# Kernel optimization log

Measured on AMD Instinct MI355X. Metric: run time of the kernel, lower is better.

## Reference

```python
import jax, jax.numpy as jnp
import numpy as np

N = 16384      # nodes
E = 524288     # edges (avg degree 32)
D = 128        # node_dim
H = 256        # hidden_dim
C = 10         # num_classes
G = 64         # graphs in batch


def setup_inputs() -> dict:
    key = jax.random.key(0)
    ks = jax.random.split(key, 8)
    x = jax.random.normal(ks[0], (N, D), dtype=jnp.float32)
    edge_index = jax.random.randint(ks[1], (2, E), 0, N)
    batch = jnp.sort(jax.random.randint(ks[2], (N,), 0, G))
    s = 0.05
    W1 = jax.random.normal(ks[3], (D, H), dtype=jnp.float32) * s
    b1 = jnp.zeros((H,), dtype=jnp.float32)
    W2 = jax.random.normal(ks[4], (H, H), dtype=jnp.float32) * s
    b2 = jnp.zeros((H,), dtype=jnp.float32)
    Wc = jax.random.normal(ks[5], (H, C), dtype=jnp.float32) * s
    bc = jnp.zeros((C,), dtype=jnp.float32)
    return {"x": x, "edge_index": edge_index, "batch": batch,
            "W1": W1, "b1": b1, "W2": W2, "b2": b2, "Wc": Wc, "bc": bc}


def _adj_norm(edge_index, n, dtype):
    # dense adjacency with self-loops (duplicates collapse to 1 via .set),
    # symmetric degree normalization D^{-1/2} A D^{-1/2}
    adj = jnp.zeros((n, n), dtype=dtype)
    adj = adj.at[edge_index[0], edge_index[1]].set(1.0)
    diag = jnp.arange(n)
    adj = adj.at[diag, diag].set(1.0)
    deg = jnp.clip(adj.sum(axis=1), 1.0, None)
    dis = deg ** -0.5
    return dis[:, None] * adj * dis[None, :]


def reference(x, edge_index, batch, W1, b1, W2, b2, Wc, bc):
    n = x.shape[0]
    A = _adj_norm(edge_index, n, x.dtype)   # [n, n], same for both layers
    h = jax.nn.relu((A @ x) @ W1 + b1)      # GCN layer 1 + relu
    h = jax.nn.relu((A @ h) @ W2 + b2)      # GCN layer 2 + relu
    pooled = jax.ops.segment_sum(h, batch, num_segments=G)            # [G, H]
    counts = jax.ops.segment_sum(jnp.ones((n,), h.dtype), batch, num_segments=G)
    pooled = pooled / jnp.clip(counts, 1.0, None)[:, None]
    # dropout is identity in eval mode
    return pooled @ Wc + bc                  # [G, C]
```

## Files before the change

kernel.cpp:

```cpp
#include <hip/hip_runtime.h>
#include <hip/hip_fp16.h>

#define NN 16384
#define EE 524288
#define DDIM 128
#define HDIM 256
#define CDIM 10
#define GG 64
#define MAXD 128

typedef _Float16 h8 __attribute__((ext_vector_type(8)));
typedef float f4 __attribute__((ext_vector_type(4)));
typedef unsigned short su8 __attribute__((ext_vector_type(8)));

#define OFF_XH   0ull
#define OFF_ELL  4194304ull
#define OFF_ELLP 8388608ull
#define OFF_Y1H  16777216ull
#define OFF_H1   20971520ull
#define OFF_Y2H  29360128ull
#define OFF_DEG  37748736ull
#define OFF_DIS  37814272ull
#define OFF_POOL 37879808ull
#define OFF_CNT  37945344ull
#define OFF_WT1  37949440ull
#define OFF_WT2  38014976ull

__global__ void init_all(const float* __restrict__ x, _Float16* __restrict__ xh,
                         const float* __restrict__ W1, _Float16* __restrict__ wt1,
                         const float* __restrict__ W2, _Float16* __restrict__ wt2,
                         const int* __restrict__ ei, unsigned short* __restrict__ ell,
                         int* __restrict__ deg,
                         float* __restrict__ pooled, float* __restrict__ cnt,
                         const int* __restrict__ batch) {
    int b = blockIdx.x, t = threadIdx.x;
    if (b < 2048) {
        int i = (b * 256 + t) * 4;
        float4 v = *(const float4*)(x + i);
        _Float16 o[4] = {(_Float16)v.x, (_Float16)v.y, (_Float16)v.z, (_Float16)v.w};
        *(ushort4*)(xh + i) = *(ushort4*)o;
    } else if (b < 2176) {
        int i = (b - 2048) * 256 + t;
        int n = i / DDIM, k = i - n * DDIM;
        wt1[i] = (_Float16)W1[k * 256 + n];
    } else if (b < 2432) {
        int i = (b - 2176) * 256 + t;
        int n = i / HDIM, k = i - n * HDIM;
        wt2[i] = (_Float16)W2[k * 256 + n];
    } else if (b < 2496) {
        int r = (b - 2432) * 256 + t;
        pooled[r] = 0.0f;
        if (r < GG) {
            int lo = 0, hi = NN;
            while (lo < hi) { int m = (lo + hi) >> 1; if (batch[m] < r) lo = m + 1; else hi = m; }
            int a = lo;
            lo = 0; hi = NN;
            while (lo < hi) { int m = (lo + hi) >> 1; if (batch[m] < r + 1) lo = m + 1; else hi = m; }
            cnt[r] = (float)(lo - a);
        }
    } else {
        int e = ((b - 2496) * 256 + t) * 2;
        int2 s2 = *(const int2*)(ei + e);
        int2 d2 = *(const int2*)(ei + EE + e);
        int pos = atomicAdd(&deg[s2.x], 1) + 1;
        if (pos < MAXD) ell[s2.x * MAXD + pos] = (unsigned short)d2.x;
        pos = atomicAdd(&deg[s2.y], 1) + 1;
        if (pos < MAXD) ell[s2.y * MAXD + pos] = (unsigned short)d2.y;
    }
}

__global__ __launch_bounds__(256) void dedup_kernel(unsigned short* __restrict__ ell,
                                                    int* __restrict__ deg,
                                                    float* __restrict__ dis) {
    int row  = blockIdx.x * 4 + (threadIdx.x >> 6);
    int lane = threadIdx.x & 63;
    int d = deg[row] + 1;
    if (d > MAXD) d = MAXD;
    int c0 = (lane == 0) ? row : ell[row * MAXD + lane];
    int c1 = ell[row * MAXD + 64 + lane];
    bool k0 = lane < d;
    bool k1 = (64 + lane) < d;
    for (int j = 0; j < d - 1; j++) {
        int cj0 = __shfl(c0, j & 63, 64);
        int cj1 = __shfl(c1, j & 63, 64);
        int cj = (j < 64) ? cj0 : cj1;
        if (k0 && lane > j && c0 == cj) k0 = false;
        if (k1 && (64 + lane) > j && c1 == cj) k1 = false;
    }
    unsigned long long m0 = __ballot(k0);
    unsigned long long m1 = __ballot(k1);
    int nd = __popcll(m0) + __popcll(m1);
    unsigned long long below = (lane == 0) ? 0ull : ((~0ull) >> (64 - lane));
    int p0 = __popcll(m0 & below);
    int p1 = __popcll(m0) + __popcll(m1 & below);
    if (k0) ell[row * MAXD + p0] = (unsigned short)c0;
    if (k1) ell[row * MAXD + p1] = (unsigned short)c1;
    if (lane == 0) {
        deg[row] = nd;
        dis[row] = 1.0f / sqrtf((float)nd);
    }
}

__global__ void pack_kernel(const unsigned short* __restrict__ ell,
                            const int* __restrict__ deg, const float* __restrict__ dis,
                            unsigned* __restrict__ ellp) {
    int i = blockIdx.x * 256 + threadIdx.x;
    int row = i >> 7;
    int slot = i & 127;
    int c = ell[i] & (NN - 1);
    float w = (slot < deg[row]) ? dis[c] : 0.0f;
    _Float16 wh = (_Float16)w;
    ellp[i] = (unsigned)c | ((unsigned)(*(unsigned short*)&wh) << 16);
}

template <int COLS>
__global__ __launch_bounds__(256) void spmm_f16(const _Float16* __restrict__ src,
                                                const unsigned* __restrict__ ellp,
                                                const int* __restrict__ deg,
                                                const float* __restrict__ dis,
                                                _Float16* __restrict__ y) {
    constexpr int SEG = COLS / 8;
    constexpr int NS  = 64 / SEG;
    constexpr int ST  = 2 * NS;
    __shared__ unsigned scw[2][MAXD];
    __shared__ float red[2][ST][COLS];
    const int row0 = blockIdx.x * 2;
    const int t    = threadIdx.x;
    const int wv   = t >> 6;
    const int ri   = wv >> 1;
    const int wp   = wv & 1;
    const int lane = t & 63;
    const int sid  = lane / SEG;
    const int l    = lane % SEG;
    const int row  = row0 + ri;
    if (t < 2 * MAXD) scw[t >> 7][t & 127] = ellp[(size_t)(row0 + (t >> 7)) * MAXD + (t & 127)];
    __syncthreads();
    const int d    = deg[row];
    const int dpad = (d + ST - 1) & ~(ST - 1);

    float acc[8];
#pragma unroll
    for (int j = 0; j < 8; j++) acc[j] = 0.0f;

    const int stream = wp * NS + sid;
    unsigned ucur = scw[ri][stream];
    su8 hcur = *(const su8*)(src + (size_t)(ucur & 0xFFFF) * COLS + l * 8);
    for (int k = stream; k < dpad; k += ST) {
        const int kn = k + ST;
        unsigned unext = 0;
        su8 hnext;
        if (kn < dpad) {
            unext = scw[ri][kn];
            hnext = *(const su8*)(src + (size_t)(unext & 0xFFFF) * COLS + l * 8);
        }
        unsigned short wb = (unsigned short)(ucur >> 16);
        float wgt = (float)(*(_Float16*)&wb);
#pragma unroll
        for (int j = 0; j < 8; j++) {
            unsigned short hb = hcur[j];
            acc[j] = fmaf(wgt, (float)(*(_Float16*)&hb), acc[j]);
        }
        ucur = unext;
        hcur = hnext;
    }
    *(f4*)&red[ri][stream][l * 8]     = (f4){acc[0], acc[1], acc[2], acc[3]};
    *(f4*)&red[ri][stream][l * 8 + 4] = (f4){acc[4], acc[5], acc[6], acc[7]};
    __syncthreads();
    if (COLS == 256) {
        float s0 = 0.0f, s1 = 0.0f;
#pragma unroll
        for (int q = 0; q < ST; q++) { s0 += red[0][q][t]; s1 += red[1][q][t]; }
        y[(size_t)row0 * COLS + t]       = (_Float16)(dis[row0] * s0);
        y[(size_t)(row0 + 1) * COLS + t] = (_Float16)(dis[row0 + 1] * s1);
    } else {
        int rr = t >> 7, c = t & 127;
        float s = 0.0f;
#pragma unroll
        for (int q = 0; q < ST; q++) s += red[rr][q][c];
        y[(size_t)(row0 + rr) * COLS + c] = (_Float16)(dis[row0 + rr] * s);
    }
}

#define ASTR 40
#define BSTR 40

#define MFMA_PROLOG                                                            \
    const int r0 = blockIdx.x * 128;                                           \
    const int c0 = blockIdx.y * 64;                                            \
    const int t = threadIdx.x;                                                 \
    const int lane = t & 63, wv = t >> 6;                                      \
    const int wm = wv >> 1, wn = wv & 1;                                       \
    const int qm = lane & 15, qk = lane >> 4;                                  \
    f4 acc[4][2];                                                              \
    _Pragma("unroll") for (int i = 0; i < 4; i++)                              \
        _Pragma("unroll") for (int j = 0; j < 2; j++)                          \
            acc[i][j] = (f4){0.f, 0.f, 0.f, 0.f};

#define MFMA_KLOOP(Aptr, Wtptr, K)                                             \
    for (int k0 = 0; k0 < K; k0 += 32) {                                       \
        __syncthreads();                                                       \
        {                                                                      \
            int r = t >> 1, ko = (t & 1) * 16;                                 \
            const su8* srcA = (const su8*)(Aptr + (size_t)(r0 + r) * K + k0 + ko); \
            su8 a0 = srcA[0], a1 = srcA[1];                                    \
            *(su8*)&As[r * ASTR + ko]     = a0;                                \
            *(su8*)&As[r * ASTR + ko + 8] = a1;                                \
            int n = t >> 2, ko2 = (t & 3) * 8;                                 \
            *(su8*)&Bs[n * BSTR + ko2] =                                       \
                *(const su8*)(Wtptr + (size_t)(c0 + n) * K + k0 + ko2);        \
        }                                                                      \
        __syncthreads();                                                       \
        h8 bfr[2];                                                             \
        _Pragma("unroll") for (int j = 0; j < 2; j++)                          \
            bfr[j] = *(const h8*)&Bs[(wn * 32 + j * 16 + qm) * BSTR + qk * 8]; \
        _Pragma("unroll") for (int i = 0; i < 4; i++) {                        \
            h8 afr = *(const h8*)&As[(wm * 64 + i * 16 + qm) * ASTR + qk * 8]; \
            _Pragma("unroll") for (int j = 0; j < 2; j++)                      \
                acc[i][j] = __builtin_amdgcn_mfma_f32_16x16x32_f16(            \
                    afr, bfr[j], acc[i][j], 0, 0, 0);                          \
        }                                                                      \
    }

template <int K>
__global__ __launch_bounds__(256) void gemm_mfma_f16(
        const _Float16* __restrict__ A, const _Float16* __restrict__ Wt,
        const float* __restrict__ bias, _Float16* __restrict__ H) {
    __shared__ __align__(16) _Float16 As[128 * ASTR];
    __shared__ __align__(16) _Float16 Bs[64 * BSTR];
    __shared__ __align__(16) _Float16 Cs[128 * 72];
    MFMA_PROLOG
    MFMA_KLOOP(A, Wt, K)

    float bv[2];
#pragma unroll
    for (int j = 0; j < 2; j++) bv[j] = bias[c0 + wn * 32 + j * 16 + qm];
#pragma unroll
    for (int i = 0; i < 4; i++)
#pragma unroll
        for (int j = 0; j < 2; j++) {
            int lc = wn * 32 + j * 16 + qm;
#pragma unroll
            for (int rr = 0; rr < 4; rr++) {
                int lr = wm * 64 + i * 16 + qk * 4 + rr;
                Cs[lr * 72 + lc] = (_Float16)fmaxf(acc[i][j][rr] + bv[j], 0.0f);
            }
        }
    __syncthreads();
    {
        int r = t >> 1, half_ = t & 1;
        _Float16* dst = H + (size_t)(r0 + r) * 256 + c0 + half_ * 32;
        const _Float16* srcc = &Cs[r * 72 + half_ * 32];
#pragma unroll
        for (int q = 0; q < 4; q++)
            *(su8*)(dst + q * 8) = *(const su8*)(srcc + q * 8);
    }
}

#define NG 8
template <int K>
__global__ __launch_bounds__(256) void gemm_mfma_pool(
        const _Float16* __restrict__ A, const _Float16* __restrict__ Wt,
        const float* __restrict__ bias, const int* __restrict__ batch,
        float* __restrict__ pooled) {
    __shared__ __align__(16) _Float16 As[128 * ASTR];
    __shared__ __align__(16) _Float16 Bs[64 * BSTR];
    __shared__ float pools[NG][68];
    __shared__ int sb[128];
    MFMA_PROLOG
    if (t < 128) sb[t] = batch[r0 + t];
    for (int i = t; i < NG * 68; i += 256) ((float*)pools)[i] = 0.0f;
    MFMA_KLOOP(A, Wt, K)

    float bv[2];
#pragma unroll
    for (int j = 0; j < 2; j++) bv[j] = bias[c0 + wn * 32 + j * 16 + qm];
    __syncthreads();
    const int g0 = sb[0];
#pragma unroll
    for (int i = 0; i < 4; i++)
#pragma unroll
        for (int j = 0; j < 2; j++) {
            int lc = wn * 32 + j * 16 + qm;
#pragma unroll
            for (int rr = 0; rr < 4; rr++) {
                int lr = wm * 64 + i * 16 + qk * 4 + rr;
                int gi = min(sb[lr] - g0, NG - 1);
                float v = fmaxf(acc[i][j][rr] + bv[j], 0.0f);
                atomicAdd(&pools[gi][lc], v);
            }
        }
    __syncthreads();
    const int ng = min(sb[127] - g0 + 1, NG);
    for (int i2 = t; i2 < ng * 64; i2 += 256) {
        int gi = i2 >> 6, c = i2 & 63;
        float v = pools[gi][c];
        if (v != 0.0f) atomicAdd(&pooled[(g0 + gi) * 256 + c0 + c], v);
    }
}

__global__ void head_kernel(const float* __restrict__ pooled,
                            const float* __restrict__ cnt,
                            const float* __restrict__ Wc,
                            const float* __restrict__ bc,
                            float* __restrict__ out) {
    int g = blockIdx.x;
    int l = threadIdx.x;
    float inv = 1.0f / fmaxf(cnt[g], 1.0f);
    float acc[CDIM];
#pragma unroll
    for (int c = 0; c < CDIM; c++) acc[c] = 0.0f;
    for (int t = l; t < 256; t += 64) {
        float pv = pooled[g * 256 + t] * inv;
#pragma unroll
        for (int c = 0; c < CDIM; c++) acc[c] = fmaf(pv, Wc[t * CDIM + c], acc[c]);
    }
#pragma unroll
    for (int c = 0; c < CDIM; c++) {
        float v = acc[c];
        for (int off = 32; off > 0; off >>= 1) v += __shfl_down(v, off, 64);
        if (l == 0) out[g * CDIM + c] = v + bc[c];
    }
}

extern "C" void kernel_launch(void* const* d_in, const int* in_sizes, int n_in,
                              void* d_out, int out_size, void* d_ws, size_t ws_size,
                              hipStream_t stream) {
    const float* x  = (const float*)d_in[0];
    const int*   ei = (const int*)d_in[1];
    const int*   batch = (const int*)d_in[2];
    const float* W1 = (const float*)d_in[3];
    const float* b1 = (const float*)d_in[4];
    const float* W2 = (const float*)d_in[5];
    const float* b2 = (const float*)d_in[6];
    const float* Wc = (const float*)d_in[7];
    const float* bc = (const float*)d_in[8];
    float* out = (float*)d_out;

    char* ws = (char*)d_ws;
    _Float16* xh   = (_Float16*)(ws + OFF_XH);
    unsigned short* ell = (unsigned short*)(ws + OFF_ELL);
    unsigned* ellp = (unsigned*)(ws + OFF_ELLP);
    _Float16* y1h  = (_Float16*)(ws + OFF_Y1H);
    _Float16* h1   = (_Float16*)(ws + OFF_H1);
    _Float16* y2h  = (_Float16*)(ws + OFF_Y2H);
    int*   deg     = (int*)(ws + OFF_DEG);
    float* dis     = (float*)(ws + OFF_DIS);
    float* pooled  = (float*)(ws + OFF_POOL);
    float* cnt     = (float*)(ws + OFF_CNT);
    _Float16* wt1  = (_Float16*)(ws + OFF_WT1);
    _Float16* wt2  = (_Float16*)(ws + OFF_WT2);

    hipMemsetAsync(deg, 0, NN * sizeof(int), stream);
    init_all<<<3520, 256, 0, stream>>>(x, xh, W1, wt1, W2, wt2, ei, ell, deg,
                                       pooled, cnt, batch);
    dedup_kernel<<<NN / 4, 256, 0, stream>>>(ell, deg, dis);
    pack_kernel<<<(NN * MAXD) / 256, 256, 0, stream>>>(ell, deg, dis, ellp);
    spmm_f16<DDIM><<<NN / 2, 256, 0, stream>>>(xh, ellp, deg, dis, y1h);
    {
        dim3 grid(NN / 128, 256 / 64);
        gemm_mfma_f16<DDIM><<<grid, 256, 0, stream>>>(y1h, wt1, b1, h1);
    }
    spmm_f16<HDIM><<<NN / 2, 256, 0, stream>>>(h1, ellp, deg, dis, y2h);
    {
        dim3 grid(NN / 128, 256 / 64);
        gemm_mfma_pool<HDIM><<<grid, 256, 0, stream>>>(y2h, wt2, b2, batch, pooled);
    }
    head_kernel<<<GG, 64, 0, stream>>>(pooled, cnt, Wc, bc, out);
}
```

Before: 217.0 us.

## Fuse sparse aggregation with MFMA GEMM per layer into single kernels

Each GCN layer's sparse gather (SpMM) and its dense MFMA GEMM now run in one kernel. Each 512-thread block gathers 32 aggregated rows into shared memory, then multiplies them by the full weight matrix and applies bias and ReLU. Layer 2 also fuses the mean-pool atomics. This removes the y1h/y2h intermediate round-trips through global memory and two kernel launches. In exchange, the gather changes from a two-wave, software-pipelined scheme to one wave per row with shuffle reductions and no prefetch, and every block reloads the full weight matrix.

```diff
diff --git a/kernel.cpp b/kernel.cpp
--- a/kernel.cpp
+++ b/kernel.cpp
@@ -16,15 +16,13 @@
 #define OFF_XH   0ull
 #define OFF_ELL  4194304ull
 #define OFF_ELLP 8388608ull
-#define OFF_Y1H  16777216ull
-#define OFF_H1   20971520ull
-#define OFF_Y2H  29360128ull
-#define OFF_DEG  37748736ull
-#define OFF_DIS  37814272ull
-#define OFF_POOL 37879808ull
-#define OFF_CNT  37945344ull
-#define OFF_WT1  37949440ull
-#define OFF_WT2  38014976ull
+#define OFF_H1   16777216ull
+#define OFF_DEG  25165824ull
+#define OFF_DIS  25231360ull
+#define OFF_POOL 25296896ull
+#define OFF_CNT  25362432ull
+#define OFF_WT1  25366528ull
+#define OFF_WT2  25432064ull
 
 __global__ void init_all(const float* __restrict__ x, _Float16* __restrict__ xh,
                          const float* __restrict__ W1, _Float16* __restrict__ wt1,
@@ -113,188 +111,179 @@
     ellp[i] = (unsigned)c | ((unsigned)(*(unsigned short*)&wh) << 16);
 }
 
-template <int COLS>
-__global__ __launch_bounds__(256) void spmm_f16(const _Float16* __restrict__ src,
-                                                const unsigned* __restrict__ ellp,
-                                                const int* __restrict__ deg,
-                                                const float* __restrict__ dis,
-                                                _Float16* __restrict__ y) {
-    constexpr int SEG = COLS / 8;
+template <int KK, int YSTR, int RPW>
+__device__ __forceinline__ void gather_rows(const _Float16* __restrict__ src,
+                                            const unsigned* __restrict__ ellp,
+                                            const int* __restrict__ deg,
+                                            const float* __restrict__ dis,
+                                            _Float16* ytile, int r0, int t) {
+    constexpr int SEG = KK / 8;
     constexpr int NS  = 64 / SEG;
-    constexpr int ST  = 2 * NS;
-    __shared__ unsigned scw[2][MAXD];
-    __shared__ float red[2][ST][COLS];
-    const int row0 = blockIdx.x * 2;
-    const int t    = threadIdx.x;
-    const int wv   = t >> 6;
-    const int ri   = wv >> 1;
-    const int wp   = wv & 1;
-    const int lane = t & 63;
-    const int sid  = lane / SEG;
-    const int l    = lane % SEG;
-    const int row  = row0 + ri;
-    if (t < 2 * MAXD) scw[t >> 7][t & 127] = ellp[(size_t)(row0 + (t >> 7)) * MAXD + (t & 127)];
+    const int wv = t >> 6, lane = t & 63;
+    const int sid = lane / SEG, l = lane % SEG;
+    for (int rr = 0; rr < RPW; rr++) {
+        const int rowl = wv * RPW + rr;
+        const int row = r0 + rowl;
+        unsigned c0 = ellp[row * MAXD + lane];
+        unsigned c1 = ellp[row * MAXD + 64 + lane];
+        const int d = deg[row];
+        const int dpad = (d + NS - 1) & ~(NS - 1);
+        float acc[8];
+#pragma unroll
+        for (int j = 0; j < 8; j++) acc[j] = 0.0f;
+        for (int k = sid; k < dpad; k += NS) {
+            unsigned ua = __shfl(c0, k & 63, 64);
+            unsigned ub = __shfl(c1, k & 63, 64);
+            unsigned u = (k < 64) ? ua : ub;
+            unsigned short wb = (unsigned short)(u >> 16);
+            float wgt = (float)(*(_Float16*)&wb);
+            su8 hv = *(const su8*)(src + (size_t)(u & 0xFFFF) * KK + l * 8);
+#pragma unroll
+            for (int j = 0; j < 8; j++) {
+                unsigned short hb = hv[j];
+                acc[j] = fmaf(wgt, (float)(*(_Float16*)&hb), acc[j]);
+            }
+        }
+        if (SEG == 16) {
+#pragma unroll
+            for (int j = 0; j < 8; j++) acc[j] += __shfl_xor(acc[j], 16, 64);
+        }
+#pragma unroll
+        for (int j = 0; j < 8; j++) acc[j] += __shfl_xor(acc[j], 32, 64);
+        if (lane < SEG) {
+            float dr = dis[row];
+            _Float16 o[8];
+#pragma unroll
+            for (int j = 0; j < 8; j++) o[j] = (_Float16)(dr * acc[j]);
+            *(su8*)&ytile[rowl * YSTR + l * 8] = *(su8*)o;
+        }
+    }
+}
+
+#define BSTR 40
+
+__global__ __launch_bounds__(512) void fused_layer1(
+        const _Float16* __restrict__ xh, const unsigned* __restrict__ ellp,
+        const int* __restrict__ deg, const float* __restrict__ dis,
+        const _Float16* __restrict__ Wt, const float* __restrict__ bias,
+        _Float16* __restrict__ H) {
+    __shared__ __align__(16) _Float16 ytile[32 * 136];
+    __shared__ __align__(16) _Float16 Bs[256 * BSTR];
+    const int r0 = blockIdx.x * 32;
+    const int t = threadIdx.x;
+    gather_rows<DDIM, 136, 4>(xh, ellp, deg, dis, ytile, r0, t);
+
+    const int lane = t & 63, wv = t >> 6;
+    const int wm = wv >> 2, wn = wv & 3;
+    const int qm = lane & 15, qk = lane >> 4;
+    f4 acc[4];
+#pragma unroll
+    for (int j = 0; j < 4; j++) acc[j] = (f4){0.f, 0.f, 0.f, 0.f};
+
+    for (int k0 = 0; k0 < DDIM; k0 += 32) {
+        __syncthreads();
+        {
+            int n = t >> 1, ko = (t & 1) * 16;
+            *(su8*)&Bs[n * BSTR + ko]     = *(const su8*)(Wt + (size_t)n * DDIM + k0 + ko);
+            *(su8*)&Bs[n * BSTR + ko + 8] = *(const su8*)(Wt + (size_t)n * DDIM + k0 + ko + 8);
+        }
+        __syncthreads();
+        h8 afr = *(const h8*)&ytile[(wm * 16 + qm) * 136 + k0 + qk * 8];
+#pragma unroll
+        for (int j = 0; j < 4; j++) {
+            h8 bfr = *(const h8*)&Bs[(wn * 64 + j * 16 + qm) * BSTR + qk * 8];
+            acc[j] = __builtin_amdgcn_mfma_f32_16x16x32_f16(afr, bfr, acc[j], 0, 0, 0);
+        }
+    }
+
+    float bv[4];
+#pragma unroll
+    for (int j = 0; j < 4; j++) bv[j] = bias[wn * 64 + j * 16 + qm];
+
+#pragma unroll
+    for (int pass = 0; pass < 2; pass++) {
+        __syncthreads();
+        if ((wn >> 1) == pass) {
+            int lc = (wn & 1) * 64;
+#pragma unroll
+            for (int j = 0; j < 4; j++) {
+#pragma unroll
+                for (int rr = 0; rr < 4; rr++) {
+                    int lr = wm * 16 + qk * 4 + rr;
+                    ytile[lr * 136 + lc + j * 16 + qm] =
+                        (_Float16)fmaxf(acc[j][rr] + bv[j], 0.0f);
+                }
+            }
+        }
+        __syncthreads();
+        {
+            int row = t >> 4, cg = (t & 15) * 8;
+            *(su8*)(H + (size_t)(r0 + row) * 256 + pass * 128 + cg) =
+                *(const su8*)&ytile[row * 136 + cg];
+        }
+    }
+}
+
+#define NG 8
+__global__ __launch_bounds__(512) void fused_layer2(
+        const _Float16* __restrict__ h1, const unsigned* __restrict__ ellp,
+        const int* __restrict__ deg, const float* __restrict__ dis,
+        const _Float16* __restrict__ Wt, const float* __restrict__ bias,
+        const int* __restrict__ batch, float* __restrict__ pooled) {
+    __shared__ __align__(16) _Float16 ytile[32 * 264];
+    __shared__ __align__(16) _Float16 Bs[256 * BSTR];
+    __shared__ float pools[NG * 264];
+    __shared__ int sb[32];
+    const int r0 = blockIdx.x * 32;
+    const int t = threadIdx.x;
+    if (t < 32) sb[t] = batch[r0 + t];
+    for (int i = t; i < NG * 264; i += 512) pools[i] = 0.0f;
+    gather_rows<HDIM, 264, 4>(h1, ellp, deg, dis, ytile, r0, t);
+
+    const int lane = t & 63, wv = t >> 6;
+    const int wm = wv >> 2, wn = wv & 3;
+    const int qm = lane & 15, qk = lane >> 4;
+    f4 acc[4];
+#pragma unroll
+    for (int j = 0; j < 4; j++) acc[j] = (f4){0.f, 0.f, 0.f, 0.f};
+
+    for (int k0 = 0; k0 < HDIM; k0 += 32) {
+        __syncthreads();
+        {
+            int n = t >> 1, ko = (t & 1) * 16;
+            *(su8*)&Bs[n * BSTR + ko]     = *(const su8*)(Wt + (size_t)n * HDIM + k0 + ko);
+            *(su8*)&Bs[n * BSTR + ko + 8] = *(const su8*)(Wt + (size_t)n * HDIM + k0 + ko + 8);
+        }
+        __syncthreads();
+        h8 afr = *(const h8*)&ytile[(wm * 16 + qm) * 264 + k0 + qk * 8];
+#pragma unroll
+        for (int j = 0; j < 4; j++) {
+            h8 bfr = *(const h8*)&Bs[(wn * 64 + j * 16 + qm) * BSTR + qk * 8];
+            acc[j] = __builtin_amdgcn_mfma_f32_16x16x32_f16(afr, bfr, acc[j], 0, 0, 0);
+        }
+    }
+
+    float bv[4];
+#pragma unroll
+    for (int j = 0; j < 4; j++) bv[j] = bias[wn * 64 + j * 16 + qm];
+    const int g0 = sb[0];
+#pragma unroll
+    for (int j = 0; j < 4; j++) {
+        int lc = wn * 64 + j * 16 + qm;
+#pragma unroll
+        for (int rr = 0; rr < 4; rr++) {
+            int lr = wm * 16 + qk * 4 + rr;
+            int gi = min(sb[lr] - g0, NG - 1);
+            float v = fmaxf(acc[j][rr] + bv[j], 0.0f);
+            atomicAdd(&pools[gi * 264 + lc], v);
+        }
+    }
     __syncthreads();
-    const int d    = deg[row];
-    const int dpad = (d + ST - 1) & ~(ST - 1);
-
-    float acc[8];
-#pragma unroll
-    for (int j = 0; j < 8; j++) acc[j] = 0.0f;
-
-    const int stream = wp * NS + sid;
-    unsigned ucur = scw[ri][stream];
-    su8 hcur = *(const su8*)(src + (size_t)(ucur & 0xFFFF) * COLS + l * 8);
-    for (int k = stream; k < dpad; k += ST) {
-        const int kn = k + ST;
-        unsigned unext = 0;
-        su8 hnext;
-        if (kn < dpad) {
-            unext = scw[ri][kn];
-            hnext = *(const su8*)(src + (size_t)(unext & 0xFFFF) * COLS + l * 8);
-        }
-        unsigned short wb = (unsigned short)(ucur >> 16);
-        float wgt = (float)(*(_Float16*)&wb);
-#pragma unroll
-        for (int j = 0; j < 8; j++) {
-            unsigned short hb = hcur[j];
-            acc[j] = fmaf(wgt, (float)(*(_Float16*)&hb), acc[j]);
-        }
-        ucur = unext;
-        hcur = hnext;
-    }
-    *(f4*)&red[ri][stream][l * 8]     = (f4){acc[0], acc[1], acc[2], acc[3]};
-    *(f4*)&red[ri][stream][l * 8 + 4] = (f4){acc[4], acc[5], acc[6], acc[7]};
-    __syncthreads();
-    if (COLS == 256) {
-        float s0 = 0.0f, s1 = 0.0f;
-#pragma unroll
-        for (int q = 0; q < ST; q++) { s0 += red[0][q][t]; s1 += red[1][q][t]; }
-        y[(size_t)row0 * COLS + t]       = (_Float16)(dis[row0] * s0);
-        y[(size_t)(row0 + 1) * COLS + t] = (_Float16)(dis[row0 + 1] * s1);
-    } else {
-        int rr = t >> 7, c = t & 127;
-        float s = 0.0f;
-#pragma unroll
-        for (int q = 0; q < ST; q++) s += red[rr][q][c];
-        y[(size_t)(row0 + rr) * COLS + c] = (_Float16)(dis[row0 + rr] * s);
-    }
-}
-
-#define ASTR 40
-#define BSTR 40
-
-#define MFMA_PROLOG                                                            \
-    const int r0 = blockIdx.x * 128;                                           \
-    const int c0 = blockIdx.y * 64;                                            \
-    const int t = threadIdx.x;                                                 \
-    const int lane = t & 63, wv = t >> 6;                                      \
-    const int wm = wv >> 1, wn = wv & 1;                                       \
-    const int qm = lane & 15, qk = lane >> 4;                                  \
-    f4 acc[4][2];                                                              \
-    _Pragma("unroll") for (int i = 0; i < 4; i++)                              \
-        _Pragma("unroll") for (int j = 0; j < 2; j++)                          \
-            acc[i][j] = (f4){0.f, 0.f, 0.f, 0.f};
-
-#define MFMA_KLOOP(Aptr, Wtptr, K)                                             \
-    for (int k0 = 0; k0 < K; k0 += 32) {                                       \
-        __syncthreads();                                                       \
-        {                                                                      \
-            int r = t >> 1, ko = (t & 1) * 16;                                 \
-            const su8* srcA = (const su8*)(Aptr + (size_t)(r0 + r) * K + k0 + ko); \
-            su8 a0 = srcA[0], a1 = srcA[1];                                    \
-            *(su8*)&As[r * ASTR + ko]     = a0;                                \
-            *(su8*)&As[r * ASTR + ko + 8] = a1;                                \
-            int n = t >> 2, ko2 = (t & 3) * 8;                                 \
-            *(su8*)&Bs[n * BSTR + ko2] =                                       \
-                *(const su8*)(Wtptr + (size_t)(c0 + n) * K + k0 + ko2);        \
-        }                                                                      \
-        __syncthreads();                                                       \
-        h8 bfr[2];                                                             \
-        _Pragma("unroll") for (int j = 0; j < 2; j++)                          \
-            bfr[j] = *(const h8*)&Bs[(wn * 32 + j * 16 + qm) * BSTR + qk * 8]; \
-        _Pragma("unroll") for (int i = 0; i < 4; i++) {                        \
-            h8 afr = *(const h8*)&As[(wm * 64 + i * 16 + qm) * ASTR + qk * 8]; \
-            _Pragma("unroll") for (int j = 0; j < 2; j++)                      \
-                acc[i][j] = __builtin_amdgcn_mfma_f32_16x16x32_f16(            \
-                    afr, bfr[j], acc[i][j], 0, 0, 0);                          \
-        }                                                                      \
-    }
-
-template <int K>
-__global__ __launch_bounds__(256) void gemm_mfma_f16(
-        const _Float16* __restrict__ A, const _Float16* __restrict__ Wt,
-        const float* __restrict__ bias, _Float16* __restrict__ H) {
-    __shared__ __align__(16) _Float16 As[128 * ASTR];
-    __shared__ __align__(16) _Float16 Bs[64 * BSTR];
-    __shared__ __align__(16) _Float16 Cs[128 * 72];
-    MFMA_PROLOG
-    MFMA_KLOOP(A, Wt, K)
-
-    float bv[2];
-#pragma unroll
-    for (int j = 0; j < 2; j++) bv[j] = bias[c0 + wn * 32 + j * 16 + qm];
-#pragma unroll
-    for (int i = 0; i < 4; i++)
-#pragma unroll
-        for (int j = 0; j < 2; j++) {
-            int lc = wn * 32 + j * 16 + qm;
-#pragma unroll
-            for (int rr = 0; rr < 4; rr++) {
-                int lr = wm * 64 + i * 16 + qk * 4 + rr;
-                Cs[lr * 72 + lc] = (_Float16)fmaxf(acc[i][j][rr] + bv[j], 0.0f);
-            }
-        }
-    __syncthreads();
-    {
-        int r = t >> 1, half_ = t & 1;
-        _Float16* dst = H + (size_t)(r0 + r) * 256 + c0 + half_ * 32;
-        const _Float16* srcc = &Cs[r * 72 + half_ * 32];
-#pragma unroll
-        for (int q = 0; q < 4; q++)
-            *(su8*)(dst + q * 8) = *(const su8*)(srcc + q * 8);
-    }
-}
-
-#define NG 8
-template <int K>
-__global__ __launch_bounds__(256) void gemm_mfma_pool(
-        const _Float16* __restrict__ A, const _Float16* __restrict__ Wt,
-        const float* __restrict__ bias, const int* __restrict__ batch,
-        float* __restrict__ pooled) {
-    __shared__ __align__(16) _Float16 As[128 * ASTR];
-    __shared__ __align__(16) _Float16 Bs[64 * BSTR];
-    __shared__ float pools[NG][68];
-    __shared__ int sb[128];
-    MFMA_PROLOG
-    if (t < 128) sb[t] = batch[r0 + t];
-    for (int i = t; i < NG * 68; i += 256) ((float*)pools)[i] = 0.0f;
-    MFMA_KLOOP(A, Wt, K)
-
-    float bv[2];
-#pragma unroll
-    for (int j = 0; j < 2; j++) bv[j] = bias[c0 + wn * 32 + j * 16 + qm];
-    __syncthreads();
-    const int g0 = sb[0];
-#pragma unroll
-    for (int i = 0; i < 4; i++)
-#pragma unroll
-        for (int j = 0; j < 2; j++) {
-            int lc = wn * 32 + j * 16 + qm;
-#pragma unroll
-            for (int rr = 0; rr < 4; rr++) {
-                int lr = wm * 64 + i * 16 + qk * 4 + rr;
-                int gi = min(sb[lr] - g0, NG - 1);
-                float v = fmaxf(acc[i][j][rr] + bv[j], 0.0f);
-                atomicAdd(&pools[gi][lc], v);
-            }
-        }
-    __syncthreads();
-    const int ng = min(sb[127] - g0 + 1, NG);
-    for (int i2 = t; i2 < ng * 64; i2 += 256) {
-        int gi = i2 >> 6, c = i2 & 63;
-        float v = pools[gi][c];
-        if (v != 0.0f) atomicAdd(&pooled[(g0 + gi) * 256 + c0 + c], v);
+    const int ng = min(sb[31] - g0 + 1, NG);
+    for (int i2 = t; i2 < ng * 256; i2 += 512) {
+        int gi = i2 >> 8, c = i2 & 255;
+        float v = pools[gi * 264 + c];
+        if (v != 0.0f) atomicAdd(&pooled[(g0 + gi) * 256 + c], v);
     }
 }
 
@@ -340,9 +329,7 @@
     _Float16* xh   = (_Float16*)(ws + OFF_XH);
     unsigned short* ell = (unsigned short*)(ws + OFF_ELL);
     unsigned* ellp = (unsigned*)(ws + OFF_ELLP);
-    _Float16* y1h  = (_Float16*)(ws + OFF_Y1H);
     _Float16* h1   = (_Float16*)(ws + OFF_H1);
-    _Float16* y2h  = (_Float16*)(ws + OFF_Y2H);
     int*   deg     = (int*)(ws + OFF_DEG);
     float* dis     = (float*)(ws + OFF_DIS);
     float* pooled  = (float*)(ws + OFF_POOL);
@@ -355,15 +342,8 @@
                                        pooled, cnt, batch);
     dedup_kernel<<<NN / 4, 256, 0, stream>>>(ell, deg, dis);
     pack_kernel<<<(NN * MAXD) / 256, 256, 0, stream>>>(ell, deg, dis, ellp);
-    spmm_f16<DDIM><<<NN / 2, 256, 0, stream>>>(xh, ellp, deg, dis, y1h);
-    {
-        dim3 grid(NN / 128, 256 / 64);
-        gemm_mfma_f16<DDIM><<<grid, 256, 0, stream>>>(y1h, wt1, b1, h1);
-    }
-    spmm_f16<HDIM><<<NN / 2, 256, 0, stream>>>(h1, ellp, deg, dis, y2h);
-    {
-        dim3 grid(NN / 128, 256 / 64);
-        gemm_mfma_pool<HDIM><<<grid, 256, 0, stream>>>(y2h, wt2, b2, batch, pooled);
-    }
+    fused_layer1<<<NN / 32, 512, 0, stream>>>(xh, ellp, deg, dis, wt1, b1, h1);
+    fused_layer2<<<NN / 32, 512, 0, stream>>>(h1, ellp, deg, dis, wt2, b2,
+                                              batch, pooled);
     head_kernel<<<GG, 64, 0, stream>>>(pooled, cnt, Wc, bc, out);
 }
```

After: 222.6 us. 1.03x slower.
